# Kernel optimization log

Measured on AMD Instinct MI355X. Metric: run time of the kernel, lower is better.

The kernel has to match this reference:

```python
import jax, jax.numpy as jnp
import numpy as np
from jax import lax

THRESH = 0.8
LENS = 0.4
DECAY = 0.2
LOG_SIG_MIN, LOG_SIG_MAX = -20.0, 2.0
WINS = 15

@jax.custom_vjp
def act_fun(x):
    return (x > THRESH).astype(x.dtype)

def _act_fwd(x):
    return act_fun(x), x

def _act_bwd(x, g):
    return (g * (jnp.abs(x - THRESH) < LENS).astype(g.dtype),)

act_fun.defvjp(_act_fwd, _act_bwd)

B, NIN, HID, NACT = 2048, 512, 1024, 32

def _xavier(key, out_d, in_d):
    lim = jnp.sqrt(6.0 / (in_d + out_d)).astype(jnp.float32)
    return jax.random.uniform(key, (out_d, in_d), jnp.float32, -lim, lim)

def setup_inputs() -> dict:
    key = jax.random.key(0)
    ks = jax.random.split(key, 12)
    inp = {
        'state': jax.random.normal(ks[0], (B, 5, NIN), jnp.float32),
        'w1': _xavier(ks[1], HID, NIN), 'b1': jnp.zeros((HID,), jnp.float32),
        'w2': _xavier(ks[2], HID, NIN), 'b2': jnp.zeros((HID,), jnp.float32),
        'w3': _xavier(ks[3], HID, NIN), 'b3': jnp.zeros((HID,), jnp.float32),
        'wl': _xavier(ks[4], 1, 3), 'bl': jnp.zeros((1,), jnp.float32),
        'w11': _xavier(ks[5], HID, 4 * HID), 'b11': jnp.zeros((HID,), jnp.float32),
        'w12': _xavier(ks[6], HID, HID), 'b12': jnp.zeros((HID,), jnp.float32),
        'w21': _xavier(ks[7], HID, 4 * HID), 'b21': jnp.zeros((HID,), jnp.float32),
        'w22': _xavier(ks[8], HID, HID), 'b22': jnp.zeros((HID,), jnp.float32),
        'wm': _xavier(ks[9], NACT, HID), 'bm': jnp.zeros((NACT,), jnp.float32),
        'ws': _xavier(ks[10], NACT, HID), 'bs': jnp.zeros((NACT,), jnp.float32),
    }
    return inp

def _policy_forward(state, w1, b1, w2, b2, w3, b3, wl, bl,
                    w11, b11, w12, b12, w21, b21, w22, b22, wm, bm, ws, bs):
    batch = state.shape[0]
    hid = w1.shape[0]
    seq = jnp.repeat(state, 3, axis=1)
    mem0 = jnp.zeros((batch, hid, 4), state.dtype)
    sp0 = jnp.zeros((batch, hid, 4), state.dtype)

    def step(carry, x_t):
        mem, spike = carry
        i1 = x_t @ w1.T + b1  # [B, HID]
        i2 = x_t @ w2.T + b2
        i3 = x_t @ w3.T + b3
        inner = jnp.einsum('bck,k->bc', mem[:, :, :3], wl[0]) + bl[0]
        inp_all = jnp.stack([i1, i2, i3, inner], axis=-1)  # [B, HID, 4]
        mem1 = mem * DECAY * (1.0 - spike) + inp_all
        sp1 = act_fun(mem1)
        return (mem1, sp1), sp1

    _, spikes = lax.scan(step, (mem0, sp0), jnp.swapaxes(seq, 0, 1))  # [T,B,HID,4]
    spikes = jnp.transpose(spikes, (1, 0, 2, 3)).reshape(batch, WINS, hid * 4)
    x = jnp.mean(spikes, axis=1)  # [B, 4*HID]

    x1 = jax.nn.relu(x @ w11.T + b11)
    x1 = jax.nn.relu(x1 @ w12.T + b12)
    mean = x1 @ wm.T + bm

    x2 = jax.nn.relu(x @ w21.T + b21)
    x2 = jax.nn.relu(x2 @ w22.T + b22)
    log_std = jnp.clip(x2 @ ws.T + bs, LOG_SIG_MIN, LOG_SIG_MAX)
    return mean, log_std

def reference(state, w1, b1, w2, b2, w3, b3, wl, bl,
              w11, b11, w12, b12, w21, b21, w22, b22, wm, bm, ws, bs):
    return _policy_forward(state, w1, b1, w2, b2, w3, b3, wl, bl,
                           w11, b11, w12, b12, w21, b21, w22, b22, wm, bm, ws, bs)
```

## Files before the change

kernel.cpp:

```cpp
#include <hip/hip_runtime.h>
#include <cstddef>
#include <cstdint>

#define THRESH 0.8f
#define DECAY  0.2f

typedef unsigned short ushort_t;
typedef __attribute__((ext_vector_type(8))) short bf16x8;
typedef __attribute__((ext_vector_type(4))) float f32x4;

__device__ __forceinline__ ushort_t f2bf(float f) {
    union { float f; unsigned u; } v; v.f = f;
    unsigned r = v.u + 0x7FFFu + ((v.u >> 16) & 1u);
    return (ushort_t)(r >> 16);
}
__device__ __forceinline__ float bf2f(ushort_t h) {
    union { unsigned u; float f; } v; v.u = ((unsigned)h) << 16;
    return v.f;
}
__device__ __forceinline__ float blo(unsigned u) {
    union { unsigned x; float f; } v; v.x = u << 16; return v.f;
}
__device__ __forceinline__ float bhi(unsigned u) {
    union { unsigned x; float f; } v; v.x = u & 0xFFFF0000u; return v.f;
}

__device__ __forceinline__ void gload16(const void* g, void* l) {
    __builtin_amdgcn_global_load_lds(
        (const __attribute__((address_space(1))) void*)g,
        (__attribute__((address_space(3))) void*)l,
        16, 0, 0);
}

template <int NSPLIT>
__global__ __launch_bounds__(512) void mfma_gemm512(
    const ushort_t* __restrict__ Ah, const ushort_t* __restrict__ Al,
    const ushort_t* __restrict__ Wh, const ushort_t* __restrict__ Wl,
    const float* __restrict__ bias, float* __restrict__ C,
    int N, int K, int lda, int ldw, int ldc, int aHalfOff,
    size_t sliceStride)
{
    constexpr int NS = (NSPLIT > 1) ? 2 : 1;
    __shared__ ushort_t sA[NS][128 * 32];
    __shared__ ushort_t sW[NS][128 * 32];

    const int t = threadIdx.x;
    const int mBase = blockIdx.x * 128;
    const int nBase = blockIdx.y * 128;
    const int kOff = blockIdx.z * K;
    const int aOff = (2 * nBase >= N) ? aHalfOff : 0;
    float* Cz = C + (size_t)blockIdx.z * sliceStride;

    const int lane = t & 63;
    const int wv = t >> 6;
    const int wm = (wv & 1) * 64;
    const int wn = (wv >> 1) * 32;
    const int fr = lane & 15;
    const int fq = lane >> 4;

    const int r0 = t >> 2;
    const int cc = (t & 3) * 8;

    f32x4 acc[4][2];
#pragma unroll
    for (int i = 0; i < 4; i++)
#pragma unroll
        for (int j = 0; j < 2; j++) {
            f32x4 z = {0.f, 0.f, 0.f, 0.f};
            acc[i][j] = z;
        }

    for (int k0 = 0; k0 < K; k0 += 32) {
        const int lin = t * 8;
        gload16(&Ah[(size_t)(mBase + r0) * lda + aOff + kOff + k0 + cc], &sA[0][lin]);
        gload16(&Wh[(size_t)(nBase + r0) * ldw + kOff + k0 + cc], &sW[0][lin]);
        if (NS == 2) {
            gload16(&Al[(size_t)(mBase + r0) * lda + aOff + kOff + k0 + cc], &sA[1][lin]);
            gload16(&Wl[(size_t)(nBase + r0) * ldw + kOff + k0 + cc], &sW[1][lin]);
        }
        __syncthreads();

        bf16x8 af[4][NS], wf[2][NS];
#pragma unroll
        for (int s = 0; s < NS; s++) {
#pragma unroll
            for (int i = 0; i < 4; i++)
                af[i][s] = *(const bf16x8*)&sA[s][(wm + i * 16 + fr) * 32 + fq * 8];
#pragma unroll
            for (int j = 0; j < 2; j++)
                wf[j][s] = *(const bf16x8*)&sW[s][(wn + j * 16 + fr) * 32 + fq * 8];
        }
#pragma unroll
        for (int i = 0; i < 4; i++)
#pragma unroll
            for (int j = 0; j < 2; j++) {
                acc[i][j] = __builtin_amdgcn_mfma_f32_16x16x32_bf16(af[i][0], wf[j][0], acc[i][j], 0, 0, 0);
                if (NSPLIT >= 3) {
                    acc[i][j] = __builtin_amdgcn_mfma_f32_16x16x32_bf16(af[i][0], wf[j][1], acc[i][j], 0, 0, 0);
                    acc[i][j] = __builtin_amdgcn_mfma_f32_16x16x32_bf16(af[i][1], wf[j][0], acc[i][j], 0, 0, 0);
                }
            }
        __syncthreads();
    }

#pragma unroll
    for (int j = 0; j < 2; j++) {
        const int col = nBase + wn + j * 16 + fr;
        const float bv = bias ? bias[col] : 0.f;
#pragma unroll
        for (int i = 0; i < 4; i++)
#pragma unroll
            for (int r = 0; r < 4; r++) {
                const int row = mBase + wm + i * 16 + fq * 4 + r;
                Cz[(size_t)row * ldc + col] = acc[i][j][r] + bv;
            }
    }
}

template <int S>
__global__ __launch_bounds__(256) void reduce_relu(
    const float* __restrict__ part, const float* __restrict__ bias,
    ushort_t* __restrict__ out, int N, size_t MN)
{
    const size_t i4 = (size_t)blockIdx.x * 256 + threadIdx.x;
    const size_t e = i4 * 4;
    if (e >= MN) return;
    float4 a = *(const float4*)&part[e];
#pragma unroll
    for (int s = 1; s < S; s++) {
        const float4 b = *(const float4*)&part[s * MN + e];
        a.x += b.x; a.y += b.y; a.z += b.z; a.w += b.w;
    }
    const int n = (int)(e & (size_t)(N - 1));
    const float4 bv = *(const float4*)&bias[n];
    ushort4 o;
    o.x = f2bf(fmaxf(a.x + bv.x, 0.f));
    o.y = f2bf(fmaxf(a.y + bv.y, 0.f));
    o.z = f2bf(fmaxf(a.z + bv.z, 0.f));
    o.w = f2bf(fmaxf(a.w + bv.w, 0.f));
    *(ushort4*)&out[e] = o;
}

__global__ __launch_bounds__(256) void recur_kernel(
    const float* __restrict__ cur, const float* __restrict__ wl,
    const float* __restrict__ bl, ushort_t* __restrict__ x)
{
    const int idx = blockIdx.x * 256 + threadIdx.x;
    const int b = idx >> 10, c = idx & 1023;
    const float wl0 = wl[0], wl1 = wl[1], wl2 = wl[2], bl0 = bl[0];
    float m0 = 0, m1 = 0, m2 = 0, m3 = 0;
    float s0 = 0, s1 = 0, s2 = 0, s3 = 0;
#pragma unroll
    for (int f = 0; f < 5; f++) {
        const float* p = cur + (size_t)(b * 5 + f) * 3072 + c;
        const float i1 = p[0], i2 = p[1024], i3 = p[2048];
#pragma unroll
        for (int rep = 0; rep < 3; rep++) {
            const float inner = m0 * wl0 + m1 * wl1 + m2 * wl2 + bl0;
            const float n0 = i1 + ((m0 > THRESH) ? 0.f : DECAY * m0);
            const float n1 = i2 + ((m1 > THRESH) ? 0.f : DECAY * m1);
            const float n2 = i3 + ((m2 > THRESH) ? 0.f : DECAY * m2);
            const float n3 = inner + ((m3 > THRESH) ? 0.f : DECAY * m3);
            m0 = n0; m1 = n1; m2 = n2; m3 = n3;
            s0 += (n0 > THRESH) ? 1.f : 0.f;
            s1 += (n1 > THRESH) ? 1.f : 0.f;
            s2 += (n2 > THRESH) ? 1.f : 0.f;
            s3 += (n3 > THRESH) ? 1.f : 0.f;
        }
    }
    const float inv = 1.f / 15.f;
    ushort4 o;
    o.x = f2bf(s0 * inv); o.y = f2bf(s1 * inv);
    o.z = f2bf(s2 * inv); o.w = f2bf(s3 * inv);
    *(ushort4*)&x[(size_t)b * 4096 + c * 4] = o;
}

__device__ __forceinline__ void do_split(const float4* src, ushort4* hi,
                                         ushort4* lo, int i) {
    const float4 v = src[i];
    ushort4 h, l;
    h.x = f2bf(v.x); l.x = f2bf(v.x - bf2f(h.x));
    h.y = f2bf(v.y); l.y = f2bf(v.y - bf2f(h.y));
    h.z = f2bf(v.z); l.z = f2bf(v.z - bf2f(h.z));
    h.w = f2bf(v.w); l.w = f2bf(v.w - bf2f(h.w));
    hi[i] = h; lo[i] = l;
}
__device__ __forceinline__ void do_cvt(const float4* src, ushort4* dst, int i) {
    const float4 v = src[i];
    ushort4 h;
    h.x = f2bf(v.x); h.y = f2bf(v.y); h.z = f2bf(v.z); h.w = f2bf(v.w);
    dst[i] = h;
}

__global__ __launch_bounds__(256) void prep_kernel(
    const float* __restrict__ state,
    const float* __restrict__ w1, const float* __restrict__ w2,
    const float* __restrict__ w3,
    const float* __restrict__ w11, const float* __restrict__ w21,
    const float* __restrict__ w12, const float* __restrict__ w22,
    const float* __restrict__ b1, const float* __restrict__ b2,
    const float* __restrict__ b3, const float* __restrict__ b11,
    const float* __restrict__ b21, const float* __restrict__ b12,
    const float* __restrict__ b22,
    ushort_t* __restrict__ sh, ushort_t* __restrict__ sl,
    ushort_t* __restrict__ wh123, ushort_t* __restrict__ wl123,
    ushort_t* __restrict__ w1b, ushort_t* __restrict__ w2b,
    float* __restrict__ b123, float* __restrict__ bb1, float* __restrict__ bb2)
{
    const int bid = blockIdx.x;
    const int t = threadIdx.x;
    if (bid < 5120) {
        do_split((const float4*)state, (ushort4*)sh, (ushort4*)sl, bid * 256 + t);
    } else if (bid < 5632) {
        do_split((const float4*)w1, (ushort4*)wh123, (ushort4*)wl123,
                 (bid - 5120) * 256 + t);
    } else if (bid < 6144) {
        do_split((const float4*)w2, (ushort4*)(wh123 + 524288),
                 (ushort4*)(wl123 + 524288), (bid - 5632) * 256 + t);
    } else if (bid < 6656) {
        do_split((const float4*)w3, (ushort4*)(wh123 + 1048576),
                 (ushort4*)(wl123 + 1048576), (bid - 6144) * 256 + t);
    } else if (bid < 10752) {
        do_cvt((const float4*)w11, (ushort4*)w1b, (bid - 6656) * 256 + t);
    } else if (bid < 14848) {
        do_cvt((const float4*)w21, (ushort4*)(w1b + 4194304), (bid - 10752) * 256 + t);
    } else if (bid < 15872) {
        do_cvt((const float4*)w12, (ushort4*)w2b, (bid - 14848) * 256 + t);
    } else if (bid < 16896) {
        do_cvt((const float4*)w22, (ushort4*)(w2b + 1048576), (bid - 15872) * 256 + t);
    } else {
        const int i = (bid - 16896) * 256 + t;
        if (i < 1024) {
            b123[i] = b1[i]; b123[1024 + i] = b2[i]; b123[2048 + i] = b3[i];
            bb1[i] = b11[i]; bb1[1024 + i] = b21[i];
            bb2[i] = b12[i]; bb2[1024 + i] = b22[i];
        }
    }
}

__global__ __launch_bounds__(256) void head_kernel(
    const ushort_t* __restrict__ h, const float* __restrict__ wm,
    const float* __restrict__ bm, const float* __restrict__ ws,
    const float* __restrict__ bs, float* __restrict__ out)
{
    const int t = threadIdx.x;
    const int branch = blockIdx.x >> 8;
    const int n = t & 31;
    const int b = (blockIdx.x & 255) * 8 + (t >> 5);
    const ushort_t* hr = h + (size_t)b * 2048 + branch * 1024;
    const float* wr = (branch ? ws : wm) + (size_t)n * 1024;
    float s = 0.f;
#pragma unroll 4
    for (int k = 0; k < 1024; k += 8) {
        const uint4 hv = *(const uint4*)&hr[k];
        const float4 w0 = *(const float4*)&wr[k];
        const float4 w1 = *(const float4*)&wr[k + 4];
        s += blo(hv.x) * w0.x + bhi(hv.x) * w0.y
           + blo(hv.y) * w0.z + bhi(hv.y) * w0.w
           + blo(hv.z) * w1.x + bhi(hv.z) * w1.y
           + blo(hv.w) * w1.z + bhi(hv.w) * w1.w;
    }
    s += (branch ? bs : bm)[n];
    if (branch) s = fminf(fmaxf(s, -20.f), 2.f);
    out[(size_t)branch * 65536 + (size_t)b * 32 + n] = s;
}

extern "C" void kernel_launch(void* const* d_in, const int* in_sizes, int n_in,
                              void* d_out, int out_size, void* d_ws, size_t ws_size,
                              hipStream_t stream)
{
    const float* state = (const float*)d_in[0];
    const float* w1  = (const float*)d_in[1];  const float* b1  = (const float*)d_in[2];
    const float* w2  = (const float*)d_in[3];  const float* b2  = (const float*)d_in[4];
    const float* w3  = (const float*)d_in[5];  const float* b3  = (const float*)d_in[6];
    const float* wl  = (const float*)d_in[7];  const float* bl  = (const float*)d_in[8];
    const float* w11 = (const float*)d_in[9];  const float* b11 = (const float*)d_in[10];
    const float* w12 = (const float*)d_in[11]; const float* b12 = (const float*)d_in[12];
    const float* w21 = (const float*)d_in[13]; const float* b21 = (const float*)d_in[14];
    const float* w22 = (const float*)d_in[15]; const float* b22 = (const float*)d_in[16];
    const float* wm  = (const float*)d_in[17]; const float* bm  = (const float*)d_in[18];
    const float* ws  = (const float*)d_in[19]; const float* bs  = (const float*)d_in[20];
    float* out = (float*)d_out;

    char* wp = (char*)d_ws;
    float*    cur   = (float*)wp;     wp += (size_t)10240 * 3072 * 4;
    ushort_t* sh    = (ushort_t*)wp;  wp += (size_t)10240 * 512 * 2;
    ushort_t* sl    = (ushort_t*)wp;  wp += (size_t)10240 * 512 * 2;
    ushort_t* wh123 = (ushort_t*)wp;  wp += (size_t)3072 * 512 * 2;
    ushort_t* wl123 = (ushort_t*)wp;  wp += (size_t)3072 * 512 * 2;
    ushort_t* xb    = (ushort_t*)wp;  wp += (size_t)2048 * 4096 * 2;
    ushort_t* w1b   = (ushort_t*)wp;  wp += (size_t)2048 * 4096 * 2;
    ushort_t* w2b   = (ushort_t*)wp;  wp += (size_t)2048 * 1024 * 2;
    ushort_t* h1    = (ushort_t*)wp;  wp += (size_t)2048 * 2048 * 2;
    ushort_t* h2    = (ushort_t*)wp;  wp += (size_t)2048 * 2048 * 2;
    float*    b123  = (float*)wp;     wp += 3072 * 4;
    float*    bb1   = (float*)wp;     wp += 2048 * 4;
    float*    bb2   = (float*)wp;     wp += 2048 * 4;

    const size_t MN = (size_t)2048 * 2048;

    prep_kernel<<<16900, 256, 0, stream>>>(
        state, w1, w2, w3, w11, w21, w12, w22,
        b1, b2, b3, b11, b21, b12, b22,
        sh, sl, wh123, wl123, w1b, w2b, b123, bb1, bb2);

    mfma_gemm512<3><<<dim3(80, 24, 1), 512, 0, stream>>>(
        sh, sl, wh123, wl123, b123, cur, 3072, 512, 512, 512, 3072, 0, 0);

    recur_kernel<<<8192, 256, 0, stream>>>(cur, wl, bl, xb);

    mfma_gemm512<1><<<dim3(16, 16, 4), 512, 0, stream>>>(
        xb, nullptr, w1b, nullptr, nullptr, cur, 2048, 1024, 4096, 4096, 2048, 0, MN);
    reduce_relu<4><<<4096, 256, 0, stream>>>(cur, bb1, h1, 2048, MN);

    mfma_gemm512<1><<<dim3(16, 16, 2), 512, 0, stream>>>(
        h1, nullptr, w2b, nullptr, nullptr, cur, 2048, 512, 2048, 1024, 2048, 1024, MN);
    reduce_relu<2><<<4096, 256, 0, stream>>>(cur, bb2, h2, 2048, MN);

    head_kernel<<<512, 256, 0, stream>>>(h2, wm, bm, ws, bs, out);
}
```

Measured before the change: 427.1 us.

## Split GEMM kernels, swizzle LDS, enlarge MLP warp tiles, grid-stride prep/reduce

Splits the templated GEMM into a dedicated 3-pass bf16-split kernel for the input projection and a 256-thread MLP GEMM. Both kernels now use an XOR-swizzled LDS layout to avoid bank conflicts. In the MLP GEMM each wave computes a 64x64 tile, so each block reuses more operand data per load, and split-K drops from 4 to 2 for the first layer. The prep and reduce kernels now process 4 elements per thread or use grid-stride loops, cutting block counts. The trade-off is fewer blocks and more registers per thread, which lowers occupancy and parallelism.

```diff
diff --git a/kernel.cpp b/kernel.cpp
--- a/kernel.cpp
+++ b/kernel.cpp
@@ -32,17 +32,90 @@
         16, 0, 0);
 }
 
-template <int NSPLIT>
-__global__ __launch_bounds__(512) void mfma_gemm512(
+__global__ __launch_bounds__(512) void cur_gemm512(
     const ushort_t* __restrict__ Ah, const ushort_t* __restrict__ Al,
     const ushort_t* __restrict__ Wh, const ushort_t* __restrict__ Wl,
     const float* __restrict__ bias, float* __restrict__ C,
+    int K, int ldc)
+{
+    __shared__ ushort_t sA[2][128 * 32];
+    __shared__ ushort_t sW[2][128 * 32];
+
+    const int t = threadIdx.x;
+    const int mBase = blockIdx.x * 128;
+    const int nBase = blockIdx.y * 128;
+
+    const int lane = t & 63;
+    const int wv = t >> 6;
+    const int wm = (wv & 1) * 64;
+    const int wn = (wv >> 1) * 32;
+    const int fr = lane & 15;
+    const int fq = lane >> 4;
+    const int fsw = (fq ^ ((fr >> 2) & 3)) * 8;
+
+    const int r0 = t >> 2;
+    const int cSw = ((t & 3) ^ ((r0 >> 2) & 3)) * 8;
+
+    f32x4 acc[4][2];
+#pragma unroll
+    for (int i = 0; i < 4; i++)
+#pragma unroll
+        for (int j = 0; j < 2; j++) {
+            f32x4 z = {0.f, 0.f, 0.f, 0.f};
+            acc[i][j] = z;
+        }
+
+    for (int k0 = 0; k0 < K; k0 += 32) {
+        const int lin = t * 8;
+        gload16(&Ah[(size_t)(mBase + r0) * K + k0 + cSw], &sA[0][lin]);
+        gload16(&Wh[(size_t)(nBase + r0) * K + k0 + cSw], &sW[0][lin]);
+        gload16(&Al[(size_t)(mBase + r0) * K + k0 + cSw], &sA[1][lin]);
+        gload16(&Wl[(size_t)(nBase + r0) * K + k0 + cSw], &sW[1][lin]);
+        __syncthreads();
+
+        bf16x8 af[4][2], wf[2][2];
+#pragma unroll
+        for (int s = 0; s < 2; s++) {
+#pragma unroll
+            for (int i = 0; i < 4; i++)
+                af[i][s] = *(const bf16x8*)&sA[s][(wm + i * 16 + fr) * 32 + fsw];
+#pragma unroll
+            for (int j = 0; j < 2; j++)
+                wf[j][s] = *(const bf16x8*)&sW[s][(wn + j * 16 + fr) * 32 + fsw];
+        }
+#pragma unroll
+        for (int i = 0; i < 4; i++)
+#pragma unroll
+            for (int j = 0; j < 2; j++) {
+                acc[i][j] = __builtin_amdgcn_mfma_f32_16x16x32_bf16(af[i][0], wf[j][0], acc[i][j], 0, 0, 0);
+                acc[i][j] = __builtin_amdgcn_mfma_f32_16x16x32_bf16(af[i][0], wf[j][1], acc[i][j], 0, 0, 0);
+                acc[i][j] = __builtin_amdgcn_mfma_f32_16x16x32_bf16(af[i][1], wf[j][0], acc[i][j], 0, 0, 0);
+            }
+        __syncthreads();
+    }
+
+#pragma unroll
+    for (int j = 0; j < 2; j++) {
+        const int col = nBase + wn + j * 16 + fr;
+        const float bv = bias[col];
+#pragma unroll
+        for (int i = 0; i < 4; i++)
+#pragma unroll
+            for (int r = 0; r < 4; r++) {
+                const int row = mBase + wm + i * 16 + fq * 4 + r;
+                C[(size_t)row * ldc + col] = acc[i][j][r] + bv;
+            }
+    }
+}
+
+__global__ __launch_bounds__(256) void mlp_gemm256(
+    const ushort_t* __restrict__ A, const ushort_t* __restrict__ W,
+    float* __restrict__ C,
     int N, int K, int lda, int ldw, int ldc, int aHalfOff,
     size_t sliceStride)
 {
-    constexpr int NS = (NSPLIT > 1) ? 2 : 1;
-    __shared__ ushort_t sA[NS][128 * 32];
-    __shared__ ushort_t sW[NS][128 * 32];
+    __shared__ ushort_t sA[128 * 32];
+    __shared__ ushort_t sW[128 * 32];
 
     const int t = threadIdx.x;
     const int mBase = blockIdx.x * 128;
@@ -54,65 +127,53 @@
     const int lane = t & 63;
     const int wv = t >> 6;
     const int wm = (wv & 1) * 64;
-    const int wn = (wv >> 1) * 32;
+    const int wn = (wv >> 1) * 64;
     const int fr = lane & 15;
     const int fq = lane >> 4;
+    const int fsw = (fq ^ ((fr >> 2) & 3)) * 8;
 
     const int r0 = t >> 2;
-    const int cc = (t & 3) * 8;
-
-    f32x4 acc[4][2];
+    const int cSw = ((t & 3) ^ ((r0 >> 2) & 3)) * 8;
+
+    f32x4 acc[4][4];
 #pragma unroll
     for (int i = 0; i < 4; i++)
 #pragma unroll
-        for (int j = 0; j < 2; j++) {
+        for (int j = 0; j < 4; j++) {
             f32x4 z = {0.f, 0.f, 0.f, 0.f};
             acc[i][j] = z;
         }
 
     for (int k0 = 0; k0 < K; k0 += 32) {
-        const int lin = t * 8;
-        gload16(&Ah[(size_t)(mBase + r0) * lda + aOff + kOff + k0 + cc], &sA[0][lin]);
-        gload16(&Wh[(size_t)(nBase + r0) * ldw + kOff + k0 + cc], &sW[0][lin]);
-        if (NS == 2) {
-            gload16(&Al[(size_t)(mBase + r0) * lda + aOff + kOff + k0 + cc], &sA[1][lin]);
-            gload16(&Wl[(size_t)(nBase + r0) * ldw + kOff + k0 + cc], &sW[1][lin]);
-        }
+        gload16(&A[(size_t)(mBase + r0) * lda + aOff + kOff + k0 + cSw], &sA[t * 8]);
+        gload16(&A[(size_t)(mBase + 64 + r0) * lda + aOff + kOff + k0 + cSw], &sA[2048 + t * 8]);
+        gload16(&W[(size_t)(nBase + r0) * ldw + kOff + k0 + cSw], &sW[t * 8]);
+        gload16(&W[(size_t)(nBase + 64 + r0) * ldw + kOff + k0 + cSw], &sW[2048 + t * 8]);
         __syncthreads();
 
-        bf16x8 af[4][NS], wf[2][NS];
-#pragma unroll
-        for (int s = 0; s < NS; s++) {
-#pragma unroll
-            for (int i = 0; i < 4; i++)
-                af[i][s] = *(const bf16x8*)&sA[s][(wm + i * 16 + fr) * 32 + fq * 8];
-#pragma unroll
-            for (int j = 0; j < 2; j++)
-                wf[j][s] = *(const bf16x8*)&sW[s][(wn + j * 16 + fr) * 32 + fq * 8];
+        bf16x8 af[4], wf[4];
+#pragma unroll
+        for (int i = 0; i < 4; i++) {
+            af[i] = *(const bf16x8*)&sA[(wm + i * 16 + fr) * 32 + fsw];
+            wf[i] = *(const bf16x8*)&sW[(wn + i * 16 + fr) * 32 + fsw];
         }
 #pragma unroll
         for (int i = 0; i < 4; i++)
 #pragma unroll
-            for (int j = 0; j < 2; j++) {
-                acc[i][j] = __builtin_amdgcn_mfma_f32_16x16x32_bf16(af[i][0], wf[j][0], acc[i][j], 0, 0, 0);
-                if (NSPLIT >= 3) {
-                    acc[i][j] = __builtin_amdgcn_mfma_f32_16x16x32_bf16(af[i][0], wf[j][1], acc[i][j], 0, 0, 0);
-                    acc[i][j] = __builtin_amdgcn_mfma_f32_16x16x32_bf16(af[i][1], wf[j][0], acc[i][j], 0, 0, 0);
-                }
-            }
+            for (int j = 0; j < 4; j++)
+                acc[i][j] = __builtin_amdgcn_mfma_f32_16x16x32_bf16(af[i], wf[j], acc[i][j], 0, 0, 0);
         __syncthreads();
     }
 
 #pragma unroll
-    for (int j = 0; j < 2; j++) {
+    for (int j = 0; j < 4; j++) {
         const int col = nBase + wn + j * 16 + fr;
-        const float bv = bias ? bias[col] : 0.f;
 #pragma unroll
         for (int i = 0; i < 4; i++)
 #pragma unroll
             for (int r = 0; r < 4; r++) {
                 const int row = mBase + wm + i * 16 + fq * 4 + r;
-                Cz[(size_t)row * ldc + col] = acc[i][j][r] + bv;
+                Cz[(size_t)row * ldc + col] = acc[i][j][r];
             }
     }
 }
@@ -122,23 +183,23 @@
     const float* __restrict__ part, const float* __restrict__ bias,
     ushort_t* __restrict__ out, int N, size_t MN)
 {
-    const size_t i4 = (size_t)blockIdx.x * 256 + threadIdx.x;
-    const size_t e = i4 * 4;
-    if (e >= MN) return;
-    float4 a = *(const float4*)&part[e];
-#pragma unroll
-    for (int s = 1; s < S; s++) {
-        const float4 b = *(const float4*)&part[s * MN + e];
-        a.x += b.x; a.y += b.y; a.z += b.z; a.w += b.w;
-    }
-    const int n = (int)(e & (size_t)(N - 1));
-    const float4 bv = *(const float4*)&bias[n];
-    ushort4 o;
-    o.x = f2bf(fmaxf(a.x + bv.x, 0.f));
-    o.y = f2bf(fmaxf(a.y + bv.y, 0.f));
-    o.z = f2bf(fmaxf(a.z + bv.z, 0.f));
-    o.w = f2bf(fmaxf(a.w + bv.w, 0.f));
-    *(ushort4*)&out[e] = o;
+    const size_t stride = (size_t)gridDim.x * 1024;
+    for (size_t e = ((size_t)blockIdx.x * 256 + threadIdx.x) * 4; e < MN; e += stride) {
+        float4 a = *(const float4*)&part[e];
+#pragma unroll
+        for (int s = 1; s < S; s++) {
+            const float4 b = *(const float4*)&part[s * MN + e];
+            a.x += b.x; a.y += b.y; a.z += b.z; a.w += b.w;
+        }
+        const int n = (int)(e & (size_t)(N - 1));
+        const float4 bv = *(const float4*)&bias[n];
+        ushort4 o;
+        o.x = f2bf(fmaxf(a.x + bv.x, 0.f));
+        o.y = f2bf(fmaxf(a.y + bv.y, 0.f));
+        o.z = f2bf(fmaxf(a.z + bv.z, 0.f));
+        o.w = f2bf(fmaxf(a.w + bv.w, 0.f));
+        *(ushort4*)&out[e] = o;
+    }
 }
 
 __global__ __launch_bounds__(256) void recur_kernel(
@@ -175,21 +236,30 @@
     *(ushort4*)&x[(size_t)b * 4096 + c * 4] = o;
 }
 
-__device__ __forceinline__ void do_split(const float4* src, ushort4* hi,
-                                         ushort4* lo, int i) {
-    const float4 v = src[i];
-    ushort4 h, l;
-    h.x = f2bf(v.x); l.x = f2bf(v.x - bf2f(h.x));
-    h.y = f2bf(v.y); l.y = f2bf(v.y - bf2f(h.y));
-    h.z = f2bf(v.z); l.z = f2bf(v.z - bf2f(h.z));
-    h.w = f2bf(v.w); l.w = f2bf(v.w - bf2f(h.w));
-    hi[i] = h; lo[i] = l;
-}
-__device__ __forceinline__ void do_cvt(const float4* src, ushort4* dst, int i) {
-    const float4 v = src[i];
-    ushort4 h;
-    h.x = f2bf(v.x); h.y = f2bf(v.y); h.z = f2bf(v.z); h.w = f2bf(v.w);
-    dst[i] = h;
+__device__ __forceinline__ void do_split4(const float4* src, ushort4* hi,
+                                          ushort4* lo, int base, int t) {
+#pragma unroll
+    for (int p = 0; p < 4; p++) {
+        const int i = base * 1024 + p * 256 + t;
+        const float4 v = src[i];
+        ushort4 h, l;
+        h.x = f2bf(v.x); l.x = f2bf(v.x - bf2f(h.x));
+        h.y = f2bf(v.y); l.y = f2bf(v.y - bf2f(h.y));
+        h.z = f2bf(v.z); l.z = f2bf(v.z - bf2f(h.z));
+        h.w = f2bf(v.w); l.w = f2bf(v.w - bf2f(h.w));
+        hi[i] = h; lo[i] = l;
+    }
+}
+__device__ __forceinline__ void do_cvt4(const float4* src, ushort4* dst,
+                                        int base, int t) {
+#pragma unroll
+    for (int p = 0; p < 4; p++) {
+        const int i = base * 1024 + p * 256 + t;
+        const float4 v = src[i];
+        ushort4 h;
+        h.x = f2bf(v.x); h.y = f2bf(v.y); h.z = f2bf(v.z); h.w = f2bf(v.w);
+        dst[i] = h;
+    }
 }
 
 __global__ __launch_bounds__(256) void prep_kernel(
@@ -209,28 +279,28 @@
 {
     const int bid = blockIdx.x;
     const int t = threadIdx.x;
-    if (bid < 5120) {
-        do_split((const float4*)state, (ushort4*)sh, (ushort4*)sl, bid * 256 + t);
-    } else if (bid < 5632) {
-        do_split((const float4*)w1, (ushort4*)wh123, (ushort4*)wl123,
-                 (bid - 5120) * 256 + t);
-    } else if (bid < 6144) {
-        do_split((const float4*)w2, (ushort4*)(wh123 + 524288),
-                 (ushort4*)(wl123 + 524288), (bid - 5632) * 256 + t);
-    } else if (bid < 6656) {
-        do_split((const float4*)w3, (ushort4*)(wh123 + 1048576),
-                 (ushort4*)(wl123 + 1048576), (bid - 6144) * 256 + t);
-    } else if (bid < 10752) {
-        do_cvt((const float4*)w11, (ushort4*)w1b, (bid - 6656) * 256 + t);
-    } else if (bid < 14848) {
-        do_cvt((const float4*)w21, (ushort4*)(w1b + 4194304), (bid - 10752) * 256 + t);
-    } else if (bid < 15872) {
-        do_cvt((const float4*)w12, (ushort4*)w2b, (bid - 14848) * 256 + t);
-    } else if (bid < 16896) {
-        do_cvt((const float4*)w22, (ushort4*)(w2b + 1048576), (bid - 15872) * 256 + t);
+    if (bid < 1280) {
+        do_split4((const float4*)state, (ushort4*)sh, (ushort4*)sl, bid, t);
+    } else if (bid < 1408) {
+        do_split4((const float4*)w1, (ushort4*)wh123, (ushort4*)wl123, bid - 1280, t);
+    } else if (bid < 1536) {
+        do_split4((const float4*)w2, (ushort4*)(wh123 + 524288),
+                  (ushort4*)(wl123 + 524288), bid - 1408, t);
+    } else if (bid < 1664) {
+        do_split4((const float4*)w3, (ushort4*)(wh123 + 1048576),
+                  (ushort4*)(wl123 + 1048576), bid - 1536, t);
+    } else if (bid < 2688) {
+        do_cvt4((const float4*)w11, (ushort4*)w1b, bid - 1664, t);
+    } else if (bid < 3712) {
+        do_cvt4((const float4*)w21, (ushort4*)(w1b + 4194304), bid - 2688, t);
+    } else if (bid < 3968) {
+        do_cvt4((const float4*)w12, (ushort4*)w2b, bid - 3712, t);
+    } else if (bid < 4224) {
+        do_cvt4((const float4*)w22, (ushort4*)(w2b + 1048576), bid - 3968, t);
     } else {
-        const int i = (bid - 16896) * 256 + t;
-        if (i < 1024) {
+#pragma unroll
+        for (int p = 0; p < 4; p++) {
+            const int i = p * 256 + t;
             b123[i] = b1[i]; b123[1024 + i] = b2[i]; b123[2048 + i] = b3[i];
             bb1[i] = b11[i]; bb1[1024 + i] = b21[i];
             bb2[i] = b12[i]; bb2[1024 + i] = b22[i];
@@ -299,23 +369,23 @@
 
     const size_t MN = (size_t)2048 * 2048;
 
-    prep_kernel<<<16900, 256, 0, stream>>>(
+    prep_kernel<<<4225, 256, 0, stream>>>(
         state, w1, w2, w3, w11, w21, w12, w22,
         b1, b2, b3, b11, b21, b12, b22,
         sh, sl, wh123, wl123, w1b, w2b, b123, bb1, bb2);
 
-    mfma_gemm512<3><<<dim3(80, 24, 1), 512, 0, stream>>>(
-        sh, sl, wh123, wl123, b123, cur, 3072, 512, 512, 512, 3072, 0, 0);
+    cur_gemm512<<<dim3(80, 24), 512, 0, stream>>>(
+        sh, sl, wh123, wl123, b123, cur, 512, 3072);
 
     recur_kernel<<<8192, 256, 0, stream>>>(cur, wl, bl, xb);
 
-    mfma_gemm512<1><<<dim3(16, 16, 4), 512, 0, stream>>>(
-        xb, nullptr, w1b, nullptr, nullptr, cur, 2048, 1024, 4096, 4096, 2048, 0, MN);
-    reduce_relu<4><<<4096, 256, 0, stream>>>(cur, bb1, h1, 2048, MN);
-
-    mfma_gemm512<1><<<dim3(16, 16, 2), 512, 0, stream>>>(
-        h1, nullptr, w2b, nullptr, nullptr, cur, 2048, 512, 2048, 1024, 2048, 1024, MN);
-    reduce_relu<2><<<4096, 256, 0, stream>>>(cur, bb2, h2, 2048, MN);
+    mlp_gemm256<<<dim3(16, 16, 2), 256, 0, stream>>>(
+        xb, w1b, cur, 2048, 2048, 4096, 4096, 2048, 0, MN);
+    reduce_relu<2><<<1024, 256, 0, stream>>>(cur, bb1, h1, 2048, MN);
+
+    mlp_gemm256<<<dim3(16, 16, 2), 256, 0, stream>>>(
+        h1, w2b, cur, 2048, 512, 2048, 1024, 2048, 1024, MN);
+    reduce_relu<2><<<1024, 256, 0, stream>>>(cur, bb2, h2, 2048, MN);
 
     head_kernel<<<512, 256, 0, stream>>>(h2, wm, bm, ws, bs, out);
 }
```

Measured after the change: 435.6 us. Within noise of the previous version (+2.0%).
